# Kernel optimization log

Measured on AMD Instinct MI355X. Metric: run time of the kernel, lower is better.

The kernel has to match this reference:

```python
import jax, jax.numpy as jnp
import numpy as np

D_MODEL = 1024
NUM_HEADS = 16
D_K = D_MODEL // NUM_HEADS
BATCH = 2
SEQ = 2048


def setup_inputs() -> dict:
    key = jax.random.key(0)
    ks = jax.random.split(key, 11)
    s = 1.0 / np.sqrt(D_MODEL)
    return {
        "query": jax.random.normal(ks[0], (BATCH, SEQ, D_MODEL), jnp.float32),
        "key_": jax.random.normal(ks[1], (BATCH, SEQ, D_MODEL), jnp.float32),
        "value": jax.random.normal(ks[2], (BATCH, SEQ, D_MODEL), jnp.float32),
        "w_q": jax.random.uniform(ks[3], (D_MODEL, D_MODEL), jnp.float32, -s, s),
        "b_q": jax.random.uniform(ks[4], (D_MODEL,), jnp.float32, -s, s),
        "w_k": jax.random.uniform(ks[5], (D_MODEL, D_MODEL), jnp.float32, -s, s),
        "b_k": jax.random.uniform(ks[6], (D_MODEL,), jnp.float32, -s, s),
        "w_v": jax.random.uniform(ks[7], (D_MODEL, D_MODEL), jnp.float32, -s, s),
        "b_v": jax.random.uniform(ks[8], (D_MODEL,), jnp.float32, -s, s),
        "w_o": jax.random.uniform(ks[9], (D_MODEL, D_MODEL), jnp.float32, -s, s),
        "b_o": jax.random.uniform(ks[10], (D_MODEL,), jnp.float32, -s, s),
    }


def reference(query, key_, value, w_q, b_q, w_k, b_k, w_v, b_v, w_o, b_o):
    B, S, D = query.shape
    H, dk = NUM_HEADS, D_K

    def proj(x, w, b):
        # torch Linear: x @ w.T + b ; reshape to (B, H, S, dk)
        return (x @ w.T + b).reshape(B, S, H, dk).transpose(0, 2, 1, 3)

    Q = proj(query, w_q, b_q)
    K = proj(key_, w_k, b_k)
    V = proj(value, w_v, b_v)

    scores = jnp.einsum("bhqd,bhkd->bhqk", Q, K) / jnp.sqrt(jnp.float32(dk))
    attn = jax.nn.softmax(scores, axis=-1)  # dropout is identity in eval
    ctx = jnp.einsum("bhqk,bhkd->bhqd", attn, V)
    ctx = ctx.transpose(0, 2, 1, 3).reshape(B, S, D)
    out = ctx @ w_o.T + b_o
    return out
```

## Files before the change

kernel.cpp:

```cpp
#include <hip/hip_runtime.h>
#include <cstdint>
#include <cstddef>

typedef unsigned short u16;
typedef short bf16x8 __attribute__((ext_vector_type(8)));
typedef unsigned short u16x8 __attribute__((ext_vector_type(8)));
typedef float f32x4 __attribute__((ext_vector_type(4)));

#define NHEAD 16
#define SEQ 2048
#define DMODEL 1024
#define BATCH 2
#define QSCALE 0.18033688011112042f

__device__ __forceinline__ float exp2_fast(float x) {
  return __builtin_amdgcn_exp2f(x);
}

__device__ __forceinline__ u16 f2bf(float f) {
  union { float f; unsigned u; } v; v.f = f;
  return (u16)((v.u + 0x7fffu + ((v.u >> 16) & 1u)) >> 16);
}

__device__ __forceinline__ int swz(int row, int colbyte) {
  return (row << 7) + (colbyte ^ ((row & 7) << 4));
}

__device__ __forceinline__ void load_lds16(const void* g, void* lds) {
  __builtin_amdgcn_global_load_lds(
      (const __attribute__((address_space(1))) unsigned int*)g,
      (__attribute__((address_space(3))) unsigned int*)lds, 16, 0, 0);
}

__global__ __launch_bounds__(256) void xconv(const float* __restrict__ i0,
                                             const float* __restrict__ i1,
                                             const float* __restrict__ i2,
                                             u16* __restrict__ o0,
                                             u16* __restrict__ o1,
                                             u16* __restrict__ o2) {
  const int y = blockIdx.y;
  const float* in = y == 0 ? i0 : y == 1 ? i1 : i2;
  u16* out = y == 0 ? o0 : y == 1 ? o1 : o2;
  int i = blockIdx.x * 256 + threadIdx.x;
  const float4* p = (const float4*)in + (size_t)i * 2;
  float4 a = p[0], b = p[1];
  u16x8 o;
  o[0] = f2bf(a.x); o[1] = f2bf(a.y); o[2] = f2bf(a.z); o[3] = f2bf(a.w);
  o[4] = f2bf(b.x); o[5] = f2bf(b.y); o[6] = f2bf(b.z); o[7] = f2bf(b.w);
  *((u16x8*)out + i) = o;
}

__global__ __launch_bounds__(256) void wconv(const float* __restrict__ i0,
                                             const float* __restrict__ i1,
                                             const float* __restrict__ i2,
                                             const float* __restrict__ i3,
                                             u16* __restrict__ o0,
                                             u16* __restrict__ o1,
                                             u16* __restrict__ o2,
                                             u16* __restrict__ o3) {
  const int y = blockIdx.y;
  const float* in = y == 0 ? i0 : y == 1 ? i1 : y == 2 ? i2 : i3;
  u16* out = y == 0 ? o0 : y == 1 ? o1 : y == 2 ? o2 : o3;
  int i = blockIdx.x * 256 + threadIdx.x;
  const float4* p = (const float4*)in + (size_t)i * 2;
  float4 a = p[0], b = p[1];
  u16x8 o;
  o[0] = f2bf(a.x); o[1] = f2bf(a.y); o[2] = f2bf(a.z); o[3] = f2bf(a.w);
  o[4] = f2bf(b.x); o[5] = f2bf(b.y); o[6] = f2bf(b.z); o[7] = f2bf(b.w);
  *((u16x8*)out + i) = o;
}

__global__ __launch_bounds__(256) void gemm_qkv(
    const u16* __restrict__ A0, const u16* __restrict__ A1, const u16* __restrict__ A2,
    const u16* __restrict__ W0, const u16* __restrict__ W1, const u16* __restrict__ W2,
    const float* __restrict__ b0, const float* __restrict__ b1, const float* __restrict__ b2,
    u16* __restrict__ C0, u16* __restrict__ C1, u16* __restrict__ C2) {
  constexpr int K = 1024;
  __shared__ u16 Ash[128 * 32];
  __shared__ u16 Bsh[128 * 32];
  const int z = blockIdx.z;
  const u16* A = z == 0 ? A0 : z == 1 ? A1 : A2;
  const u16* W = z == 0 ? W0 : z == 1 ? W1 : W2;
  const float* bias = z == 0 ? b0 : z == 1 ? b1 : b2;
  u16* C = z == 0 ? C0 : z == 1 ? C1 : C2;
  const float scale = z == 0 ? QSCALE : 1.0f;

  const int t = threadIdx.x;
  const int w = t >> 6;
  const int l = t & 63;
  const int m0 = blockIdx.y * 128;
  const int n0 = blockIdx.x * 128;
  const int wm = (w >> 1) * 64;
  const int wn = (w & 1) * 64;
  const int lr = l & 15;
  const int hi = l >> 4;
  const int lk = hi * 8;
  const int srow = l >> 2;
  const int scol = (l & 3) * 8;

  f32x4 acc[4][4] = {};

  for (int k0 = 0; k0 < K; k0 += 32) {
#pragma unroll
    for (int c = 0; c < 2; ++c) {
      int ra = (c * 4 + w) * 16 + srow;
      load_lds16(A + (size_t)(m0 + ra) * K + k0 + scol, &Ash[(c * 4 + w) * 512]);
      load_lds16(W + (size_t)(n0 + ra) * K + k0 + scol, &Bsh[(c * 4 + w) * 512]);
    }
    __syncthreads();
    bf16x8 af[4], bfr[4];
#pragma unroll
    for (int i = 0; i < 4; ++i)
      af[i] = *(const bf16x8*)&Ash[(wm + i * 16 + lr) * 32 + lk];
#pragma unroll
    for (int j = 0; j < 4; ++j)
      bfr[j] = *(const bf16x8*)&Bsh[(wn + j * 16 + lr) * 32 + lk];
#pragma unroll
    for (int i = 0; i < 4; ++i)
#pragma unroll
      for (int j = 0; j < 4; ++j)
        acc[i][j] = __builtin_amdgcn_mfma_f32_16x16x32_bf16(af[i], bfr[j], acc[i][j], 0, 0, 0);
    __syncthreads();
  }

#pragma unroll
  for (int i = 0; i < 4; ++i)
#pragma unroll
    for (int j = 0; j < 4; ++j)
#pragma unroll
      for (int r = 0; r < 4; ++r) {
        int row = m0 + wm + i * 16 + hi * 4 + r;
        int col = n0 + wn + j * 16 + lr;
        float v = (acc[i][j][r] + bias[col]) * scale;
        int b = row >> 11, s = row & 2047;
        int h = col >> 6, d = col & 63;
        C[(((size_t)(b * NHEAD + h) * SEQ + s) << 6) + d] = f2bf(v);
      }
}

__global__ __launch_bounds__(256) void gemm_o(const u16* __restrict__ A,
                                              const u16* __restrict__ W,
                                              const float* __restrict__ bias,
                                              float* __restrict__ C) {
  constexpr int K = 1024;
  __shared__ u16 Ash[64 * 32];
  __shared__ u16 Bsh[128 * 32];
  const int t = threadIdx.x;
  const int w = t >> 6;
  const int l = t & 63;
  const int m0 = blockIdx.y * 64;
  const int n0 = blockIdx.x * 128;
  const int wm = (w >> 1) * 32;
  const int wn = (w & 1) * 64;
  const int lr = l & 15;
  const int hi = l >> 4;
  const int lk = hi * 8;
  const int srow = l >> 2;
  const int scol = (l & 3) * 8;

  f32x4 acc[2][4] = {};

  for (int k0 = 0; k0 < K; k0 += 32) {
    {
      int ra = w * 16 + srow;
      load_lds16(A + (size_t)(m0 + ra) * K + k0 + scol, &Ash[w * 512]);
    }
#pragma unroll
    for (int c = 0; c < 2; ++c) {
      int rb = (c * 4 + w) * 16 + srow;
      load_lds16(W + (size_t)(n0 + rb) * K + k0 + scol, &Bsh[(c * 4 + w) * 512]);
    }
    __syncthreads();
    bf16x8 af[2], bfr[4];
#pragma unroll
    for (int i = 0; i < 2; ++i)
      af[i] = *(const bf16x8*)&Ash[(wm + i * 16 + lr) * 32 + lk];
#pragma unroll
    for (int j = 0; j < 4; ++j)
      bfr[j] = *(const bf16x8*)&Bsh[(wn + j * 16 + lr) * 32 + lk];
#pragma unroll
    for (int i = 0; i < 2; ++i)
#pragma unroll
      for (int j = 0; j < 4; ++j)
        acc[i][j] = __builtin_amdgcn_mfma_f32_16x16x32_bf16(af[i], bfr[j], acc[i][j], 0, 0, 0);
    __syncthreads();
  }

#pragma unroll
  for (int i = 0; i < 2; ++i)
#pragma unroll
    for (int j = 0; j < 4; ++j)
#pragma unroll
      for (int r = 0; r < 4; ++r) {
        int row = m0 + wm + i * 16 + hi * 4 + r;
        int col = n0 + wn + j * 16 + lr;
        C[(size_t)row * DMODEL + col] = acc[i][j][r] + bias[col];
      }
}

__global__ __launch_bounds__(256) void transpose_v(const u16* __restrict__ V,
                                                   u16* __restrict__ Vt) {
  __shared__ u16 tile[64][72];
  int st = blockIdx.x, bh = blockIdx.y;
  int t = threadIdx.x;
  {
    int s = t >> 2, part = (t & 3) * 16;
    const u16* g = V + (((size_t)bh * SEQ + st * 64 + s) << 6) + part;
    u16x8 v0 = *(const u16x8*)&g[0];
    u16x8 v1 = *(const u16x8*)&g[8];
    *(u16x8*)&tile[s][part] = v0;
    *(u16x8*)&tile[s][part + 8] = v1;
  }
  __syncthreads();
  {
    int d = t >> 2, sp = (t & 3) * 16;
    u16x8 o0, o1;
#pragma unroll
    for (int j = 0; j < 8; ++j) {
      int c0 = sp + j, c1 = sp + 8 + j;
      o0[j] = tile[(c0 & 3) * 16 + (c0 >> 2)][d];
      o1[j] = tile[(c1 & 3) * 16 + (c1 >> 2)][d];
    }
    u16* out = Vt + ((size_t)bh * 64 + d) * SEQ + st * 64 + sp;
    *(u16x8*)&out[0] = o0;
    *(u16x8*)&out[8] = o1;
  }
}

__global__ __launch_bounds__(256) void attn(const u16* __restrict__ Q,
                                            const u16* __restrict__ K,
                                            const u16* __restrict__ Vt,
                                            u16* __restrict__ ctx) {
  __shared__ u16 Qs[128 * 64];
  __shared__ u16 Ks[2][64 * 64];
  __shared__ u16 Vs[2][64 * 64];
  char* const QsB = (char*)Qs;

  const int t = threadIdx.x, w = t >> 6, l = t & 63;
  const int bh = blockIdx.y;
  const int q0 = blockIdx.x * 128;
  const int lr = l & 15, hi = l >> 4;

  const u16* Qg = Q + ((size_t)bh * SEQ + q0) * 64;
  const u16* Kg = K + (size_t)bh * SEQ * 64;
  const u16* Vg = Vt + (size_t)bh * 64 * SEQ;

#pragma unroll
  for (int i = 0; i < 4; ++i) {
    int c = i * 256 + t;
    int row = c >> 3, cb = (c & 7) * 16;
    u16x8 qv = *(const u16x8*)&Qg[row * 64 + cb / 2];
    *(u16x8*)(QsB + swz(row, cb)) = qv;
  }
  const int srow = t >> 2;
  const int scb = (t & 3) * 32;
  {
    u16x8 k0 = *(const u16x8*)&Kg[srow * 64 + scb / 2];
    u16x8 k1 = *(const u16x8*)&Kg[srow * 64 + scb / 2 + 8];
    u16x8 v0 = *(const u16x8*)&Vg[(size_t)srow * SEQ + scb / 2];
    u16x8 v1 = *(const u16x8*)&Vg[(size_t)srow * SEQ + scb / 2 + 8];
    char* KsB = (char*)Ks[0];
    char* VsB = (char*)Vs[0];
    *(u16x8*)(KsB + swz(srow, scb)) = k0;
    *(u16x8*)(KsB + swz(srow, scb + 16)) = k1;
    *(u16x8*)(VsB + swz(srow, scb)) = v0;
    *(u16x8*)(VsB + swz(srow, scb + 16)) = v1;
  }
  __syncthreads();

  bf16x8 qf[2][2];
#pragma unroll
  for (int mt = 0; mt < 2; ++mt)
#pragma unroll
    for (int ks = 0; ks < 2; ++ks)
      qf[mt][ks] = *(const bf16x8*)(QsB + swz(w * 32 + mt * 16 + lr, ks * 64 + hi * 16));

  f32x4 acc[2][4] = {};
  float lsum[2][4] = {{0.f, 0.f, 0.f, 0.f}, {0.f, 0.f, 0.f, 0.f}};

  int cur = 0;
  for (int kt = 0; kt < SEQ / 64; ++kt) {
    u16x8 nk0, nk1, nv0, nv1;
    const bool pf = (kt + 1 < SEQ / 64);
    if (pf) {
      const u16* kg = Kg + (kt + 1) * 4096;
      const u16* vg = Vg + (kt + 1) * 64;
      nk0 = *(const u16x8*)&kg[srow * 64 + scb / 2];
      nk1 = *(const u16x8*)&kg[srow * 64 + scb / 2 + 8];
      nv0 = *(const u16x8*)&vg[(size_t)srow * SEQ + scb / 2];
      nv1 = *(const u16x8*)&vg[(size_t)srow * SEQ + scb / 2 + 8];
    }

    char* const KsB = (char*)Ks[cur];
    f32x4 sc[2][4] = {};
#pragma unroll
    for (int ks = 0; ks < 2; ++ks) {
      bf16x8 kb[4];
#pragma unroll
      for (int nt = 0; nt < 4; ++nt)
        kb[nt] = *(const bf16x8*)(KsB + swz(nt * 16 + lr, ks * 64 + hi * 16));
#pragma unroll
      for (int mt = 0; mt < 2; ++mt)
#pragma unroll
        for (int nt = 0; nt < 4; ++nt)
          sc[mt][nt] = __builtin_amdgcn_mfma_f32_16x16x32_bf16(qf[mt][ks], kb[nt], sc[mt][nt], 0, 0, 0);
    }

#pragma unroll
    for (int mt = 0; mt < 2; ++mt)
#pragma unroll
      for (int r = 0; r < 4; ++r) {
        int prow = w * 32 + mt * 16 + hi * 4 + r;
        float p0 = exp2_fast(sc[mt][0][r]);
        float p1 = exp2_fast(sc[mt][1][r]);
        float p2 = exp2_fast(sc[mt][2][r]);
        float p3 = exp2_fast(sc[mt][3][r]);
        lsum[mt][r] += (p0 + p1) + (p2 + p3);
        uint2 pk;
        asm("v_cvt_pk_bf16_f32 %0, %1, %2" : "=v"(pk.x) : "v"(p0), "v"(p1));
        asm("v_cvt_pk_bf16_f32 %0, %1, %2" : "=v"(pk.y) : "v"(p2), "v"(p3));
        *(uint2*)(QsB + swz(prow, lr * 8)) = pk;
      }

    char* const VsB = (char*)Vs[cur];
#pragma unroll
    for (int ks = 0; ks < 2; ++ks) {
      bf16x8 pa[2], vb[4];
#pragma unroll
      for (int mt = 0; mt < 2; ++mt)
        pa[mt] = *(const bf16x8*)(QsB + swz(w * 32 + mt * 16 + lr, ks * 64 + hi * 16));
#pragma unroll
      for (int nt = 0; nt < 4; ++nt)
        vb[nt] = *(const bf16x8*)(VsB + swz(nt * 16 + lr, ks * 64 + hi * 16));
#pragma unroll
      for (int mt = 0; mt < 2; ++mt)
#pragma unroll
        for (int nt = 0; nt < 4; ++nt)
          acc[mt][nt] = __builtin_amdgcn_mfma_f32_16x16x32_bf16(pa[mt], vb[nt], acc[mt][nt], 0, 0, 0);
    }

    if (pf) {
      char* KsN = (char*)Ks[cur ^ 1];
      char* VsN = (char*)Vs[cur ^ 1];
      *(u16x8*)(KsN + swz(srow, scb)) = nk0;
      *(u16x8*)(KsN + swz(srow, scb + 16)) = nk1;
      *(u16x8*)(VsN + swz(srow, scb)) = nv0;
      *(u16x8*)(VsN + swz(srow, scb + 16)) = nv1;
    }
    __syncthreads();
    cur ^= 1;
  }

  const int b = bh >> 4, h = bh & 15;
#pragma unroll
  for (int mt = 0; mt < 2; ++mt)
#pragma unroll
    for (int r = 0; r < 4; ++r) {
      float s = lsum[mt][r];
      s += __shfl_xor(s, 1);
      s += __shfl_xor(s, 2);
      s += __shfl_xor(s, 4);
      s += __shfl_xor(s, 8);
      float inv = 1.0f / s;
      int srow_ = q0 + w * 32 + mt * 16 + hi * 4 + r;
#pragma unroll
      for (int nt = 0; nt < 4; ++nt) {
        int d = nt * 16 + lr;
        ctx[((size_t)(b * SEQ + srow_)) * DMODEL + h * 64 + d] =
            f2bf(acc[mt][nt][r] * inv);
      }
    }
}

extern "C" void kernel_launch(void* const* d_in, const int* in_sizes, int n_in,
                              void* d_out, int out_size, void* d_ws, size_t ws_size,
                              hipStream_t stream) {
  const float* q  = (const float*)d_in[0];
  const float* k  = (const float*)d_in[1];
  const float* v  = (const float*)d_in[2];
  const float* wq = (const float*)d_in[3];
  const float* bq = (const float*)d_in[4];
  const float* wk = (const float*)d_in[5];
  const float* bk = (const float*)d_in[6];
  const float* wv = (const float*)d_in[7];
  const float* bv = (const float*)d_in[8];
  const float* wo = (const float*)d_in[9];
  const float* bo = (const float*)d_in[10];

  const size_t XB = (size_t)4096 * 1024 * 2;
  const size_t WB = (size_t)1024 * 1024 * 2;
  char* ws = (char*)d_ws;
  u16* Xq = (u16*)(ws);
  u16* Xk = (u16*)(ws + XB);
  u16* Xv = (u16*)(ws + 2 * XB);
  u16* Wq = (u16*)(ws + 3 * XB);
  u16* Wk = (u16*)(ws + 3 * XB + WB);
  u16* Wv = (u16*)(ws + 3 * XB + 2 * WB);
  u16* Wo = (u16*)(ws + 3 * XB + 3 * WB);
  u16* Qb = (u16*)(ws + 4 * XB);
  u16* Kb = (u16*)(ws + 5 * XB);
  u16* Vb = (u16*)(ws + 6 * XB);
  u16* Vtb = Xk;
  u16* ctxb = Xq;

  xconv<<<dim3(2048, 3), 256, 0, stream>>>(q, k, v, Xq, Xk, Xv);
  wconv<<<dim3(512, 4), 256, 0, stream>>>(wq, wk, wv, wo, Wq, Wk, Wv, Wo);

  gemm_qkv<<<dim3(8, 32, 3), 256, 0, stream>>>(Xq, Xk, Xv, Wq, Wk, Wv,
                                               bq, bk, bv, Qb, Kb, Vb);

  transpose_v<<<dim3(SEQ / 64, BATCH * NHEAD), 256, 0, stream>>>(Vb, Vtb);

  attn<<<dim3(SEQ / 128, BATCH * NHEAD), 256, 0, stream>>>(Qb, Kb, Vtb, ctxb);

  gemm_o<<<dim3(8, 64), 256, 0, stream>>>(ctxb, Wo, bo, (float*)d_out);
}
```

Before: 131.6 us.

## Fuse conversions, fold V transpose into QKV GEMM, shrink attention query tile

Merges the two fp32-to-bf16 conversion kernels into one launch. Folds the V transpose into the QKV GEMM epilogue through an LDS staging tile, removing a separate kernel and a round trip of V through global memory. Halves the attention query tile to 64 rows with a remapped 1D grid, giving 1024 blocks for better occupancy and CU fill. In exchange the attention kernel reuses each K/V tile across fewer query rows, and the GEMM gains extra LDS and barriers in its V epilogue.

```diff
diff --git a/kernel.cpp b/kernel.cpp
--- a/kernel.cpp
+++ b/kernel.cpp
@@ -32,41 +32,35 @@
       (__attribute__((address_space(3))) unsigned int*)lds, 16, 0, 0);
 }
 
-__global__ __launch_bounds__(256) void xconv(const float* __restrict__ i0,
-                                             const float* __restrict__ i1,
-                                             const float* __restrict__ i2,
-                                             u16* __restrict__ o0,
-                                             u16* __restrict__ o1,
-                                             u16* __restrict__ o2) {
-  const int y = blockIdx.y;
-  const float* in = y == 0 ? i0 : y == 1 ? i1 : i2;
-  u16* out = y == 0 ? o0 : y == 1 ? o1 : o2;
-  int i = blockIdx.x * 256 + threadIdx.x;
+__global__ __launch_bounds__(256) void convall(
+    const float* __restrict__ q, const float* __restrict__ k, const float* __restrict__ v,
+    const float* __restrict__ wq, const float* __restrict__ wk,
+    const float* __restrict__ wv, const float* __restrict__ wo,
+    u16* __restrict__ Xq, u16* __restrict__ Xk, u16* __restrict__ Xv,
+    u16* __restrict__ Wq, u16* __restrict__ Wk, u16* __restrict__ Wv,
+    u16* __restrict__ Wo) {
+  int bid = blockIdx.x;
+  const float* in;
+  u16* out;
+  int local;
+  if (bid < 6144) {
+    int a = bid >> 11;
+    local = bid & 2047;
+    in = a == 0 ? q : a == 1 ? k : v;
+    out = a == 0 ? Xq : a == 1 ? Xk : Xv;
+  } else {
+    int bb = bid - 6144;
+    int a = bb >> 9;
+    local = bb & 511;
+    in = a == 0 ? wq : a == 1 ? wk : a == 2 ? wv : wo;
+    out = a == 0 ? Wq : a == 1 ? Wk : a == 2 ? Wv : Wo;
+  }
+  int i = local * 256 + threadIdx.x;
   const float4* p = (const float4*)in + (size_t)i * 2;
-  float4 a = p[0], b = p[1];
+  float4 a4 = p[0], b4 = p[1];
   u16x8 o;
-  o[0] = f2bf(a.x); o[1] = f2bf(a.y); o[2] = f2bf(a.z); o[3] = f2bf(a.w);
-  o[4] = f2bf(b.x); o[5] = f2bf(b.y); o[6] = f2bf(b.z); o[7] = f2bf(b.w);
-  *((u16x8*)out + i) = o;
-}
-
-__global__ __launch_bounds__(256) void wconv(const float* __restrict__ i0,
-                                             const float* __restrict__ i1,
-                                             const float* __restrict__ i2,
-                                             const float* __restrict__ i3,
-                                             u16* __restrict__ o0,
-                                             u16* __restrict__ o1,
-                                             u16* __restrict__ o2,
-                                             u16* __restrict__ o3) {
-  const int y = blockIdx.y;
-  const float* in = y == 0 ? i0 : y == 1 ? i1 : y == 2 ? i2 : i3;
-  u16* out = y == 0 ? o0 : y == 1 ? o1 : y == 2 ? o2 : o3;
-  int i = blockIdx.x * 256 + threadIdx.x;
-  const float4* p = (const float4*)in + (size_t)i * 2;
-  float4 a = p[0], b = p[1];
-  u16x8 o;
-  o[0] = f2bf(a.x); o[1] = f2bf(a.y); o[2] = f2bf(a.z); o[3] = f2bf(a.w);
-  o[4] = f2bf(b.x); o[5] = f2bf(b.y); o[6] = f2bf(b.z); o[7] = f2bf(b.w);
+  o[0] = f2bf(a4.x); o[1] = f2bf(a4.y); o[2] = f2bf(a4.z); o[3] = f2bf(a4.w);
+  o[4] = f2bf(b4.x); o[5] = f2bf(b4.y); o[6] = f2bf(b4.z); o[7] = f2bf(b4.w);
   *((u16x8*)out + i) = o;
 }
 
@@ -78,6 +72,7 @@
   constexpr int K = 1024;
   __shared__ u16 Ash[128 * 32];
   __shared__ u16 Bsh[128 * 32];
+  __shared__ u16 Tsh[64][137];
   const int z = blockIdx.z;
   const u16* A = z == 0 ? A0 : z == 1 ? A1 : A2;
   const u16* W = z == 0 ? W0 : z == 1 ? W1 : W2;
@@ -123,19 +118,57 @@
     __syncthreads();
   }
 
-#pragma unroll
-  for (int i = 0; i < 4; ++i)
-#pragma unroll
-    for (int j = 0; j < 4; ++j)
-#pragma unroll
-      for (int r = 0; r < 4; ++r) {
-        int row = m0 + wm + i * 16 + hi * 4 + r;
-        int col = n0 + wn + j * 16 + lr;
-        float v = (acc[i][j][r] + bias[col]) * scale;
-        int b = row >> 11, s = row & 2047;
-        int h = col >> 6, d = col & 63;
-        C[(((size_t)(b * NHEAD + h) * SEQ + s) << 6) + d] = f2bf(v);
+  if (z != 2) {
+#pragma unroll
+    for (int i = 0; i < 4; ++i)
+#pragma unroll
+      for (int j = 0; j < 4; ++j)
+#pragma unroll
+        for (int r = 0; r < 4; ++r) {
+          int row = m0 + wm + i * 16 + hi * 4 + r;
+          int col = n0 + wn + j * 16 + lr;
+          float v = (acc[i][j][r] + bias[col]) * scale;
+          int b = row >> 11, s = row & 2047;
+          int h = col >> 6, d = col & 63;
+          C[(((size_t)(b * NHEAD + h) * SEQ + s) << 6) + d] = f2bf(v);
+        }
+  } else {
+    const int b = m0 >> 11, s0 = m0 & 2047;
+    const int h0 = n0 >> 6;
+#pragma unroll
+    for (int p = 0; p < 2; ++p) {
+      if ((w & 1) == p) {
+#pragma unroll
+        for (int i = 0; i < 4; ++i)
+#pragma unroll
+          for (int j = 0; j < 4; ++j)
+#pragma unroll
+            for (int r = 0; r < 4; ++r) {
+              int rl = wm + i * 16 + hi * 4 + r;
+              int dl = j * 16 + lr;
+              Tsh[dl][rl] = f2bf(acc[i][j][r] + bias[n0 + p * 64 + dl]);
+            }
       }
+      __syncthreads();
+      {
+        int d = t >> 2, cpart = (t & 3) * 16;
+        u16* outp = C + ((size_t)(b * NHEAD + h0 + p) * 64 + d) * SEQ + s0;
+#pragma unroll
+        for (int blk = 0; blk < 2; ++blk)
+#pragma unroll
+          for (int vv = 0; vv < 2; ++vv) {
+            u16x8 o;
+#pragma unroll
+            for (int jj = 0; jj < 8; ++jj) {
+              int c = cpart + vv * 8 + jj;
+              o[jj] = Tsh[d][blk * 64 + (c & 3) * 16 + (c >> 2)];
+            }
+            *(u16x8*)&outp[blk * 64 + cpart + vv * 8] = o;
+          }
+      }
+      __syncthreads();
+    }
+  }
 }
 
 __global__ __launch_bounds__(256) void gemm_o(const u16* __restrict__ A,
@@ -198,55 +231,29 @@
       }
 }
 
-__global__ __launch_bounds__(256) void transpose_v(const u16* __restrict__ V,
-                                                   u16* __restrict__ Vt) {
-  __shared__ u16 tile[64][72];
-  int st = blockIdx.x, bh = blockIdx.y;
-  int t = threadIdx.x;
-  {
-    int s = t >> 2, part = (t & 3) * 16;
-    const u16* g = V + (((size_t)bh * SEQ + st * 64 + s) << 6) + part;
-    u16x8 v0 = *(const u16x8*)&g[0];
-    u16x8 v1 = *(const u16x8*)&g[8];
-    *(u16x8*)&tile[s][part] = v0;
-    *(u16x8*)&tile[s][part + 8] = v1;
-  }
-  __syncthreads();
-  {
-    int d = t >> 2, sp = (t & 3) * 16;
-    u16x8 o0, o1;
-#pragma unroll
-    for (int j = 0; j < 8; ++j) {
-      int c0 = sp + j, c1 = sp + 8 + j;
-      o0[j] = tile[(c0 & 3) * 16 + (c0 >> 2)][d];
-      o1[j] = tile[(c1 & 3) * 16 + (c1 >> 2)][d];
-    }
-    u16* out = Vt + ((size_t)bh * 64 + d) * SEQ + st * 64 + sp;
-    *(u16x8*)&out[0] = o0;
-    *(u16x8*)&out[8] = o1;
-  }
-}
-
 __global__ __launch_bounds__(256) void attn(const u16* __restrict__ Q,
                                             const u16* __restrict__ K,
                                             const u16* __restrict__ Vt,
                                             u16* __restrict__ ctx) {
-  __shared__ u16 Qs[128 * 64];
+  __shared__ u16 Qs[64 * 64];
   __shared__ u16 Ks[2][64 * 64];
   __shared__ u16 Vs[2][64 * 64];
   char* const QsB = (char*)Qs;
 
   const int t = threadIdx.x, w = t >> 6, l = t & 63;
-  const int bh = blockIdx.y;
-  const int q0 = blockIdx.x * 128;
   const int lr = l & 15, hi = l >> 4;
+
+  const int bid = blockIdx.x;
+  const int idx = bid >> 3;
+  const int bh = (bid & 7) * 4 + (idx >> 5);
+  const int q0 = (idx & 31) * 64;
 
   const u16* Qg = Q + ((size_t)bh * SEQ + q0) * 64;
   const u16* Kg = K + (size_t)bh * SEQ * 64;
   const u16* Vg = Vt + (size_t)bh * 64 * SEQ;
 
 #pragma unroll
-  for (int i = 0; i < 4; ++i) {
+  for (int i = 0; i < 2; ++i) {
     int c = i * 256 + t;
     int row = c >> 3, cb = (c & 7) * 16;
     u16x8 qv = *(const u16x8*)&Qg[row * 64 + cb / 2];
@@ -268,15 +275,13 @@
   }
   __syncthreads();
 
-  bf16x8 qf[2][2];
-#pragma unroll
-  for (int mt = 0; mt < 2; ++mt)
-#pragma unroll
-    for (int ks = 0; ks < 2; ++ks)
-      qf[mt][ks] = *(const bf16x8*)(QsB + swz(w * 32 + mt * 16 + lr, ks * 64 + hi * 16));
-
-  f32x4 acc[2][4] = {};
-  float lsum[2][4] = {{0.f, 0.f, 0.f, 0.f}, {0.f, 0.f, 0.f, 0.f}};
+  bf16x8 qf[2];
+#pragma unroll
+  for (int ks = 0; ks < 2; ++ks)
+    qf[ks] = *(const bf16x8*)(QsB + swz(w * 16 + lr, ks * 64 + hi * 16));
+
+  f32x4 acc[4] = {};
+  float lsum[4] = {0.f, 0.f, 0.f, 0.f};
 
   int cur = 0;
   for (int kt = 0; kt < SEQ / 64; ++kt) {
@@ -292,7 +297,7 @@
     }
 
     char* const KsB = (char*)Ks[cur];
-    f32x4 sc[2][4] = {};
+    f32x4 sc[4] = {};
 #pragma unroll
     for (int ks = 0; ks < 2; ++ks) {
       bf16x8 kb[4];
@@ -300,43 +305,35 @@
       for (int nt = 0; nt < 4; ++nt)
         kb[nt] = *(const bf16x8*)(KsB + swz(nt * 16 + lr, ks * 64 + hi * 16));
 #pragma unroll
-      for (int mt = 0; mt < 2; ++mt)
-#pragma unroll
-        for (int nt = 0; nt < 4; ++nt)
-          sc[mt][nt] = __builtin_amdgcn_mfma_f32_16x16x32_bf16(qf[mt][ks], kb[nt], sc[mt][nt], 0, 0, 0);
-    }
-
-#pragma unroll
-    for (int mt = 0; mt < 2; ++mt)
-#pragma unroll
-      for (int r = 0; r < 4; ++r) {
-        int prow = w * 32 + mt * 16 + hi * 4 + r;
-        float p0 = exp2_fast(sc[mt][0][r]);
-        float p1 = exp2_fast(sc[mt][1][r]);
-        float p2 = exp2_fast(sc[mt][2][r]);
-        float p3 = exp2_fast(sc[mt][3][r]);
-        lsum[mt][r] += (p0 + p1) + (p2 + p3);
-        uint2 pk;
-        asm("v_cvt_pk_bf16_f32 %0, %1, %2" : "=v"(pk.x) : "v"(p0), "v"(p1));
-        asm("v_cvt_pk_bf16_f32 %0, %1, %2" : "=v"(pk.y) : "v"(p2), "v"(p3));
-        *(uint2*)(QsB + swz(prow, lr * 8)) = pk;
-      }
+      for (int nt = 0; nt < 4; ++nt)
+        sc[nt] = __builtin_amdgcn_mfma_f32_16x16x32_bf16(qf[ks], kb[nt], sc[nt], 0, 0, 0);
+    }
+
+#pragma unroll
+    for (int r = 0; r < 4; ++r) {
+      int prow = w * 16 + hi * 4 + r;
+      float p0 = exp2_fast(sc[0][r]);
+      float p1 = exp2_fast(sc[1][r]);
+      float p2 = exp2_fast(sc[2][r]);
+      float p3 = exp2_fast(sc[3][r]);
+      lsum[r] += (p0 + p1) + (p2 + p3);
+      uint2 pk;
+      asm("v_cvt_pk_bf16_f32 %0, %1, %2" : "=v"(pk.x) : "v"(p0), "v"(p1));
+      asm("v_cvt_pk_bf16_f32 %0, %1, %2" : "=v"(pk.y) : "v"(p2), "v"(p3));
+      *(uint2*)(QsB + swz(prow, lr * 8)) = pk;
+    }
 
     char* const VsB = (char*)Vs[cur];
 #pragma unroll
     for (int ks = 0; ks < 2; ++ks) {
-      bf16x8 pa[2], vb[4];
-#pragma unroll
-      for (int mt = 0; mt < 2; ++mt)
-        pa[mt] = *(const bf16x8*)(QsB + swz(w * 32 + mt * 16 + lr, ks * 64 + hi * 16));
+      bf16x8 pa, vb[4];
+      pa = *(const bf16x8*)(QsB + swz(w * 16 + lr, ks * 64 + hi * 16));
 #pragma unroll
       for (int nt = 0; nt < 4; ++nt)
         vb[nt] = *(const bf16x8*)(VsB + swz(nt * 16 + lr, ks * 64 + hi * 16));
 #pragma unroll
-      for (int mt = 0; mt < 2; ++mt)
-#pragma unroll
-        for (int nt = 0; nt < 4; ++nt)
-          acc[mt][nt] = __builtin_amdgcn_mfma_f32_16x16x32_bf16(pa[mt], vb[nt], acc[mt][nt], 0, 0, 0);
+      for (int nt = 0; nt < 4; ++nt)
+        acc[nt] = __builtin_amdgcn_mfma_f32_16x16x32_bf16(pa, vb[nt], acc[nt], 0, 0, 0);
     }
 
     if (pf) {
@@ -353,23 +350,21 @@
 
   const int b = bh >> 4, h = bh & 15;
 #pragma unroll
-  for (int mt = 0; mt < 2; ++mt)
-#pragma unroll
-    for (int r = 0; r < 4; ++r) {
-      float s = lsum[mt][r];
-      s += __shfl_xor(s, 1);
-      s += __shfl_xor(s, 2);
-      s += __shfl_xor(s, 4);
-      s += __shfl_xor(s, 8);
-      float inv = 1.0f / s;
-      int srow_ = q0 + w * 32 + mt * 16 + hi * 4 + r;
-#pragma unroll
-      for (int nt = 0; nt < 4; ++nt) {
-        int d = nt * 16 + lr;
-        ctx[((size_t)(b * SEQ + srow_)) * DMODEL + h * 64 + d] =
-            f2bf(acc[mt][nt][r] * inv);
-      }
-    }
+  for (int r = 0; r < 4; ++r) {
+    float s = lsum[r];
+    s += __shfl_xor(s, 1);
+    s += __shfl_xor(s, 2);
+    s += __shfl_xor(s, 4);
+    s += __shfl_xor(s, 8);
+    float inv = 1.0f / s;
+    int srow_ = q0 + w * 16 + hi * 4 + r;
+#pragma unroll
+    for (int nt = 0; nt < 4; ++nt) {
+      int d = nt * 16 + lr;
+      ctx[((size_t)(b * SEQ + srow_)) * DMODEL + h * 64 + d] =
+          f2bf(acc[nt][r] * inv);
+    }
+  }
 }
 
 extern "C" void kernel_launch(void* const* d_in, const int* in_sizes, int n_in,
@@ -399,19 +394,16 @@
   u16* Wo = (u16*)(ws + 3 * XB + 3 * WB);
   u16* Qb = (u16*)(ws + 4 * XB);
   u16* Kb = (u16*)(ws + 5 * XB);
-  u16* Vb = (u16*)(ws + 6 * XB);
-  u16* Vtb = Xk;
+  u16* Vtb = (u16*)(ws + 6 * XB);
   u16* ctxb = Xq;
 
-  xconv<<<dim3(2048, 3), 256, 0, stream>>>(q, k, v, Xq, Xk, Xv);
-  wconv<<<dim3(512, 4), 256, 0, stream>>>(wq, wk, wv, wo, Wq, Wk, Wv, Wo);
+  convall<<<8192, 256, 0, stream>>>(q, k, v, wq, wk, wv, wo,
+                                    Xq, Xk, Xv, Wq, Wk, Wv, Wo);
 
   gemm_qkv<<<dim3(8, 32, 3), 256, 0, stream>>>(Xq, Xk, Xv, Wq, Wk, Wv,
-                                               bq, bk, bv, Qb, Kb, Vb);
-
-  transpose_v<<<dim3(SEQ / 64, BATCH * NHEAD), 256, 0, stream>>>(Vb, Vtb);
-
-  attn<<<dim3(SEQ / 128, BATCH * NHEAD), 256, 0, stream>>>(Qb, Kb, Vtb, ctxb);
+                                               bq, bk, bv, Qb, Kb, Vtb);
+
+  attn<<<1024, 256, 0, stream>>>(Qb, Kb, Vtb, ctxb);
 
   gemm_o<<<dim3(8, 64), 256, 0, stream>>>(ctxb, Wo, bo, (float*)d_out);
 }
```

Measured after the change: 151.1 us. 14.8% more time.
